# Optimization experiments

Hardware: AMD Instinct MI355X
Metric: run time of the kernel (lower is better)

Reference implementation:

```python
import jax, jax.numpy as jnp
import numpy as np

B, S, D, H, L, W, O = 4, 1024, 512, 8, 6, 64, 300
DH = D // H          # head dim = 64
R = 2 * W + 3        # rel_proj output dim = 131
EPS = 1e-6


def setup_inputs() -> dict:
    key = jax.random.key(0)
    ks = jax.random.split(key, 12)
    sc = 0.02
    x = jax.random.normal(ks[0], (B, S, D), jnp.float32)
    inp = {
        "x": x,
        "ln1_g": jnp.ones((L, D), jnp.float32),
        "ln1_b": jnp.zeros((L, D), jnp.float32),
        "qkv_w": jax.random.normal(ks[1], (L, D, 3 * D), jnp.float32) * sc,
        "qkv_b": jnp.zeros((L, 3 * D), jnp.float32),
        "rel_w": jax.random.normal(ks[2], (DH, R), jnp.float32) * sc,
        "rel_b": jnp.zeros((R,), jnp.float32),
        "ln2_g": jnp.ones((L, D), jnp.float32),
        "ln2_b": jnp.zeros((L, D), jnp.float32),
        "mlp_w1": jax.random.normal(ks[3], (L, D, 4 * D), jnp.float32) * sc,
        "mlp_b1": jnp.zeros((L, 4 * D), jnp.float32),
        "mlp_w2": jax.random.normal(ks[4], (L, 4 * D, D), jnp.float32) * sc,
        "mlp_b2": jnp.zeros((L, D), jnp.float32),
        "normf_g": jnp.ones((D,), jnp.float32),
        "normf_b": jnp.zeros((D,), jnp.float32),
        "head_w": jax.random.normal(ks[5], (D, O), jnp.float32) * sc,
        "head_b": jnp.zeros((O,), jnp.float32),
        "mask": jax.random.randint(ks[6], (B, O), 0, 2, jnp.int32),
    }
    return inp


def _layernorm(x, g, b):
    m = jnp.mean(x, axis=-1, keepdims=True)
    v = jnp.mean(jnp.square(x - m), axis=-1, keepdims=True)
    return (x - m) * jax.lax.rsqrt(v + EPS) * g + b


def _forward(x, ln1_g, ln1_b, qkv_w, qkv_b, rel_w, rel_b, ln2_g, ln2_b,
             mlp_w1, mlp_b1, mlp_w2, mlp_b2, normf_g, normf_b, head_w, head_b, mask):
    b, s, d = x.shape
    # clamped relative offsets, shifted to [0, 2W]; shape [s, s]
    ar = jnp.arange(s)
    offsets = jnp.clip(ar[None, :] - ar[:, None], -W, W) + W
    off_bh = jnp.broadcast_to(offsets[None, None], (b, H, s, s))
    scale = 1.0 / np.sqrt(D / H)  # = 1/sqrt(dh)

    def block(xc, lp):
        (l1g, l1b, qw, qb, l2g, l2b, w1, b1, w2, b2) = lp
        h = _layernorm(xc, l1g, l1b)
        qkv = (h @ qw + qb).reshape(b, s, H, 3 * DH)
        q, k, v = jnp.split(qkv, 3, axis=-1)            # [b,s,h,dh] each
        q = q.transpose(0, 2, 1, 3)                     # [b,h,s,dh]
        k = k.transpose(0, 2, 1, 3)
        v = v.transpose(0, 2, 1, 3)
        content = jnp.einsum('bhik,bhjk->bhij', q, k) * scale
        pos = q @ rel_w + rel_b                          # [b,h,s,R]
        pos_scores = jnp.take_along_axis(pos, off_bh, axis=-1)  # [b,h,s,s]
        attn = jax.nn.softmax(content + pos_scores, axis=-1)
        out = jnp.einsum('bhij,bhjk->bhik', attn, v)     # [b,h,s,dh]
        xc = xc + out.transpose(0, 2, 1, 3).reshape(b, s, d)
        h2 = _layernorm(xc, l2g, l2b)
        m = jax.nn.gelu(h2 @ w1 + b1, approximate=False) @ w2 + b2
        return xc + m, None

    layer_params = (ln1_g, ln1_b, qkv_w, qkv_b, ln2_g, ln2_b,
                    mlp_w1, mlp_b1, mlp_w2, mlp_b2)
    x, _ = jax.lax.scan(block, x, layer_params)
    x = _layernorm(x, normf_g, normf_b)[:, 0, :]         # CLS token
    logits = x @ head_w + head_b                          # [b, O]
    return jnp.where(mask == 0, -jnp.inf, logits)


def reference(x, ln1_g, ln1_b, qkv_w, qkv_b, rel_w, rel_b, ln2_g, ln2_b,
              mlp_w1, mlp_b1, mlp_w2, mlp_b2, normf_g, normf_b, head_w, head_b, mask):
    return _forward(x, ln1_g, ln1_b, qkv_w, qkv_b, rel_w, rel_b, ln2_g, ln2_b,
                    mlp_w1, mlp_b1, mlp_w2, mlp_b2, normf_g, normf_b, head_w, head_b, mask)
```

## Files before the change

### kernel.cpp

```cpp
#include <hip/hip_runtime.h>
#include <math.h>

#define B_  4
#define S_  1024
#define D_  512
#define H_  8
#define L_  6
#define W_  64
#define O_  300
#define DH_ 64
#define R_  131
#define R2_ 132

typedef __attribute__((ext_vector_type(8))) short bf16x8;
typedef __attribute__((ext_vector_type(4))) float f32x4;

#define SWZ(r) ((((r) ^ ((r) >> 3)) & 7) << 4)

__device__ __forceinline__ float gelu_f(float x) {
    return 0.5f * x * (1.0f + erff(x * 0.70710678118654752f));
}

__device__ __forceinline__ unsigned short f2bf(float f) {
    union { float f; unsigned u; } c; c.f = f;
    unsigned u = c.u;
    unsigned r = (u + 0x7fffu + ((u >> 16) & 1u)) >> 16;
    return (unsigned short)r;
}
__device__ __forceinline__ float bf2f(unsigned short u) {
    union { unsigned u; float f; } c; c.u = ((unsigned)u) << 16; return c.f;
}

__device__ __forceinline__ void gload_lds16(const void* g, void* l) {
    __builtin_amdgcn_global_load_lds(
        (const __attribute__((address_space(1))) unsigned int*)g,
        (__attribute__((address_space(3))) unsigned int*)l, 16, 0, 0);
}

__global__ __launch_bounds__(256) void ln_kernel(
    const float* __restrict__ x, const float* __restrict__ g,
    const float* __restrict__ b, unsigned short* __restrict__ y, int rows)
{
    int wave = threadIdx.x >> 6;
    int lane = threadIdx.x & 63;
    int row  = blockIdx.x * 4 + wave;
    if (row >= rows) return;
    const float* xr = x + (size_t)row * D_;
    float4 v0 = *(const float4*)(xr + lane * 4);
    float4 v1 = *(const float4*)(xr + 256 + lane * 4);

    float s = v0.x + v0.y + v0.z + v0.w + v1.x + v1.y + v1.z + v1.w;
    #pragma unroll
    for (int off = 32; off >= 1; off >>= 1) s += __shfl_xor(s, off);
    float mean = s * (1.0f / 512.0f);

    float a0 = v0.x - mean, a1 = v0.y - mean, a2 = v0.z - mean, a3 = v0.w - mean;
    float a4 = v1.x - mean, a5 = v1.y - mean, a6 = v1.z - mean, a7 = v1.w - mean;
    float vs = a0*a0 + a1*a1 + a2*a2 + a3*a3 + a4*a4 + a5*a5 + a6*a6 + a7*a7;
    #pragma unroll
    for (int off = 32; off >= 1; off >>= 1) vs += __shfl_xor(vs, off);
    float rstd = rsqrtf(vs * (1.0f / 512.0f) + 1e-6f);

    float4 g0 = *(const float4*)(g + lane * 4);
    float4 g1 = *(const float4*)(g + 256 + lane * 4);
    float4 b0 = *(const float4*)(b + lane * 4);
    float4 b1 = *(const float4*)(b + 256 + lane * 4);

    unsigned short* yr = y + (size_t)row * D_;
    ushort4 p0 = {f2bf(a0 * rstd * g0.x + b0.x), f2bf(a1 * rstd * g0.y + b0.y),
                  f2bf(a2 * rstd * g0.z + b0.z), f2bf(a3 * rstd * g0.w + b0.w)};
    ushort4 p1 = {f2bf(a4 * rstd * g1.x + b1.x), f2bf(a5 * rstd * g1.y + b1.y),
                  f2bf(a6 * rstd * g1.z + b1.z), f2bf(a7 * rstd * g1.w + b1.w)};
    *(ushort4*)(yr + lane * 4)       = p0;
    *(ushort4*)(yr + 256 + lane * 4) = p1;
}

__global__ __launch_bounds__(256) void tconv_kernel(
    const float* __restrict__ in, unsigned short* __restrict__ out, int K, int N)
{
    __shared__ float t[32][33];
    int tx = threadIdx.x & 31, ty = threadIdx.x >> 5;
    int n0 = blockIdx.x * 32, k0 = blockIdx.y * 32;
    #pragma unroll
    for (int j = 0; j < 4; ++j)
        t[ty + 8*j][tx] = in[(size_t)(k0 + ty + 8*j) * N + n0 + tx];
    __syncthreads();
    #pragma unroll
    for (int j = 0; j < 4; ++j)
        out[(size_t)(n0 + ty + 8*j) * K + k0 + tx] = f2bf(t[tx][ty + 8*j]);
}

__global__ __launch_bounds__(256) void relw_prep(
    const float* __restrict__ rel_w, unsigned short* __restrict__ relwT)
{
    for (int i = threadIdx.x; i < 144 * 64; i += 256) {
        int r = i >> 6, c = i & 63;
        relwT[i] = (r < R_) ? f2bf(rel_w[(size_t)c * R_ + r]) : (unsigned short)0;
    }
}

__global__ __launch_bounds__(256) void prep_all(
    const float* __restrict__ qkv_w, const float* __restrict__ mlp_w1,
    const float* __restrict__ mlp_w2, const float* __restrict__ rel_w,
    unsigned short* __restrict__ wTq_all, unsigned short* __restrict__ wT1_all,
    unsigned short* __restrict__ wT2_all, unsigned short* __restrict__ relwT)
{
    int bid = blockIdx.x;
    if (bid >= 16896) {
        for (int i = threadIdx.x; i < 144 * 64; i += 256) {
            int r = i >> 6, c = i & 63;
            relwT[i] = (r < R_) ? f2bf(rel_w[(size_t)c * R_ + r]) : (unsigned short)0;
        }
        return;
    }
    int l = bid / 2816, rr = bid - l * 2816;
    const float* in; unsigned short* out; int K, N, bx, by;
    if (rr < 768) {
        in = qkv_w + (size_t)l * 512 * 1536; out = wTq_all + (size_t)l * 1536 * 512;
        K = 512; N = 1536; bx = rr % 48; by = rr / 48;
    } else if (rr < 1792) {
        int r2 = rr - 768;
        in = mlp_w1 + (size_t)l * 512 * 2048; out = wT1_all + (size_t)l * 2048 * 512;
        K = 512; N = 2048; bx = r2 % 64; by = r2 / 64;
    } else {
        int r2 = rr - 1792;
        in = mlp_w2 + (size_t)l * 2048 * 512; out = wT2_all + (size_t)l * 512 * 2048;
        K = 2048; N = 512; bx = r2 % 16; by = r2 / 16;
    }
    __shared__ float t[32][33];
    int tx = threadIdx.x & 31, ty = threadIdx.x >> 5;
    int n0 = bx * 32, k0 = by * 32;
    #pragma unroll
    for (int j = 0; j < 4; ++j)
        t[ty + 8*j][tx] = in[(size_t)(k0 + ty + 8*j) * N + n0 + tx];
    __syncthreads();
    #pragma unroll
    for (int j = 0; j < 4; ++j)
        out[(size_t)(n0 + ty + 8*j) * K + k0 + tx] = f2bf(t[tx][ty + 8*j]);
}

template<int ACT, int OBF, int BM, int BN, int WM, int WN, int BK>
__global__ __launch_bounds__(256) void mfma_gemm(
    const unsigned short* __restrict__ A, const unsigned short* __restrict__ BT,
    const float* __restrict__ bias, const float* __restrict__ resid,
    void* __restrict__ Cout, int M, int N, int K)
{
    static_assert(WM * WN == 4, "4 waves");
    constexpr int MFR = BM / WM / 16;
    constexpr int NFR = BN / WN / 16;
    constexpr int TPR = BK / 8;
    constexpr int RPP = 256 / TPR;
    __shared__ __align__(16) unsigned short As[BM * BK];
    __shared__ __align__(16) unsigned short Bs[BN * BK];
    int tid  = threadIdx.x;
    int lane = tid & 63;
    int l15 = lane & 15, l4 = lane >> 4;
    int wid  = tid >> 6;
    int wave_m = (wid / WN) * (BM / WM);
    int wave_n = (wid % WN) * (BN / WN);

    int nwg = gridDim.x * gridDim.y;
    int bid0 = blockIdx.y * gridDim.x + blockIdx.x;
    int bid = (bid0 & 7) * (nwg >> 3) + (bid0 >> 3);
    int bm = (bid / gridDim.x) * BM, bn = (bid % gridDim.x) * BN;

    const f32x4 z4 = {0.f, 0.f, 0.f, 0.f};
    f32x4 acc[MFR][NFR];
    #pragma unroll
    for (int m = 0; m < MFR; ++m)
        #pragma unroll
        for (int n = 0; n < NFR; ++n) acc[m][n] = z4;

    int arow = tid / TPR;
    int acol8 = ((tid % TPR) ^ (arow & (TPR - 1))) * 8;
    const unsigned short* Ab = A  + (size_t)(bm + arow) * K + acol8;
    const unsigned short* Bb = BT + (size_t)(bn + arow) * K + acol8;
    unsigned short* Adst = As + tid * 8;
    unsigned short* Bdst = Bs + tid * 8;

    int swzA = l15 & (TPR - 1);
    const unsigned short* Afrag = As + (size_t)(wave_m + l15) * BK;
    const unsigned short* Bfrag = Bs + (size_t)(wave_n + l15) * BK;

    for (int k0 = 0; k0 < K; k0 += BK) {
        #pragma unroll
        for (int ch = 0; ch < BM / RPP; ++ch)
            gload_lds16(Ab + (size_t)ch * RPP * K + k0, Adst + ch * RPP * BK);
        #pragma unroll
        for (int ch = 0; ch < BN / RPP; ++ch)
            gload_lds16(Bb + (size_t)ch * RPP * K + k0, Bdst + ch * RPP * BK);
        __syncthreads();

        #pragma unroll
        for (int kk = 0; kk < BK / 32; ++kk) {
            int off8 = ((l4 + 4 * kk) ^ swzA) * 8;
            bf16x8 af[MFR], bfr[NFR];
            #pragma unroll
            for (int m = 0; m < MFR; ++m) af[m]  = *(const bf16x8*)(Afrag + m * 16 * BK + off8);
            #pragma unroll
            for (int n = 0; n < NFR; ++n) bfr[n] = *(const bf16x8*)(Bfrag + n * 16 * BK + off8);
            #pragma unroll
            for (int m = 0; m < MFR; ++m)
                #pragma unroll
                for (int n = 0; n < NFR; ++n)
                    acc[m][n] = __builtin_amdgcn_mfma_f32_16x16x32_bf16(af[m], bfr[n], acc[m][n], 0, 0, 0);
        }
        __syncthreads();
    }

    int r0 = bm + wave_m + (l4 * 4);
    int c0 = bn + wave_n + l15;
    #pragma unroll
    for (int m = 0; m < MFR; ++m) {
        #pragma unroll
        for (int n = 0; n < NFR; ++n) {
            int c = c0 + n * 16;
            float bv = bias[c];
            #pragma unroll
            for (int q = 0; q < 4; ++q) {
                int r = r0 + m * 16 + q;
                float v = acc[m][n][q] + bv;
                if (ACT == 1) v = gelu_f(v);
                if (resid) v += resid[(size_t)r * N + c];
                if (OBF) ((unsigned short*)Cout)[(size_t)r * N + c] = f2bf(v);
                else     ((float*)Cout)[(size_t)r * N + c] = v;
            }
        }
    }
}

__global__ __launch_bounds__(512, 2) void attn_mfma(
    const unsigned short* __restrict__ qkv,
    const unsigned short* __restrict__ relwT,
    const float* __restrict__ rel_b,
    float* __restrict__ xres)
{
    __shared__ __align__(16) unsigned char shm[49664];
    unsigned char* Klds  = shm;
    unsigned char* Vtlds = shm + 16384;
    unsigned short* pos16 = (unsigned short*)(shm + 32768);
    float* mergeO  = (float*)shm;
    float* mergeML = (float*)(shm + 17408);

    int tid = threadIdx.x, lane = tid & 63, w = tid >> 6;
    int l15 = lane & 15, l4 = lane >> 4;
    int wq = w & 3;
    int g  = w >> 2;
    int it0 = blockIdx.x * 64;
    int h = blockIdx.y, b = blockIdx.z;
    const float LOG2E = 1.4426950408889634f;
    const float SC = 0.125f * LOG2E;
    const float THR = 11.5441f;

    bf16x8 qa[2];
    {
        const unsigned short* qp = qkv + (size_t)(b * S_ + it0 + wq * 16 + l15) * 1536 + h * 192 + l4 * 8;
        qa[0] = *(const bf16x8*)(qp);
        qa[1] = *(const bf16x8*)(qp + 32);
    }

    if (g == 0) {
        #pragma unroll
        for (int n = 0; n < 9; ++n) {
            f32x4 pacc = {0.f, 0.f, 0.f, 0.f};
            #pragma unroll
            for (int ks = 0; ks < 2; ++ks) {
                bf16x8 bv = *(const bf16x8*)(relwT + (size_t)(16 * n + l15) * 64 + ks * 32 + l4 * 8);
                pacc = __builtin_amdgcn_mfma_f32_16x16x32_bf16(qa[ks], bv, pacc, 0, 0, 0);
            }
            int c = 16 * n + l15;
            if (c < R_) {
                float rb = rel_b[c];
                #pragma unroll
                for (int q = 0; q < 4; ++q)
                    pos16[(wq * 16 + l4 * 4 + q) * R2_ + c] = f2bf((pacc[q] + rb) * LOG2E);
            }
        }
    }
    __syncthreads();

    int rloc = wq * 16 + l15;
    int i_glob = it0 + rloc;
    float p_lo = bf2f(pos16[rloc * R2_ + 0]);
    float p_hi = bf2f(pos16[rloc * R2_ + 128]);

    int rf = tid >> 2, seg = tid & 3;
    int gk = rf >> 6, rr = rf & 63;
    const unsigned short* kbase = qkv + (size_t)(b * S_ + gk * 512 + rr) * 1536 + h * 192 + 64 + seg * 16;
    int kbyt = gk * 8192 + ((rr * 128 + seg * 32) ^ SWZ(rr));
    int pf = tid >> 3, seg8 = tid & 7;
    int gv = pf >> 5, pp = pf & 31;
    const unsigned short* vbase = qkv + (size_t)(b * S_ + gv * 512 + 2 * pp) * 1536 + h * 192 + 128 + seg8 * 8;
    bf16x8 kr0, kr1, vr0, vr1;
    kr0 = *(const bf16x8*)(kbase);
    kr1 = *(const bf16x8*)(kbase + 8);
    vr0 = *(const bf16x8*)(vbase);
    vr1 = *(const bf16x8*)(vbase + 1536);

    const f32x4 z4 = {0.f, 0.f, 0.f, 0.f};
    f32x4 oacc[4];
    #pragma unroll
    for (int n = 0; n < 4; ++n) oacc[n] = z4;
    float mrun_s = -INFINITY, lrun_s = 0.f;
    int wmin = it0 + wq * 16;
    unsigned char* Kw = Klds + g * 8192;
    unsigned char* Vw = Vtlds + g * 8192;

    int idx_lo = (l15 + 32 * (l4 & 1)) * 4;
    int idx_hi = idx_lo + 64;
    bool hi_n = (l4 >> 1) != 0;

    for (int t = 0; t < 8; ++t) {
        int jt0 = g * 512 + t * 64;
        __syncthreads();
        *(bf16x8*)(Klds + kbyt) = kr0;
        *(bf16x8*)(Klds + (kbyt ^ 16)) = kr1;
        #pragma unroll
        for (int i = 0; i < 8; ++i) {
            int dh = seg8 * 8 + i;
            unsigned v01 = (unsigned)(unsigned short)vr0[i] | ((unsigned)(unsigned short)vr1[i] << 16);
            *(unsigned*)(Vtlds + gv * 8192 + ((dh * 128 + pp * 4) ^ SWZ(dh))) = v01;
        }
        __syncthreads();
        if (t < 7) {
            const unsigned short* kp = kbase + (size_t)(t + 1) * 64 * 1536;
            kr0 = *(const bf16x8*)(kp);
            kr1 = *(const bf16x8*)(kp + 8);
            const unsigned short* vp = vbase + (size_t)(t + 1) * 64 * 1536;
            vr0 = *(const bf16x8*)(vp);
            vr1 = *(const bf16x8*)(vp + 1536);
        }

        f32x4 ssw[4];
        #pragma unroll
        for (int n = 0; n < 4; ++n) ssw[n] = z4;
        #pragma unroll
        for (int n = 0; n < 4; ++n) {
            int kvr = 16 * n + l15;
            #pragma unroll
            for (int ks = 0; ks < 2; ++ks) {
                bf16x8 ak = *(const bf16x8*)(Kw + ((kvr * 128 + ks * 64 + l4 * 16) ^ SWZ(kvr)));
                ssw[n] = __builtin_amdgcn_mfma_f32_16x16x32_bf16(ak, qa[ks], ssw[n], 0, 0, 0);
            }
        }

        float sv[4][4];
        bool left  = (jt0 + 63 < wmin - 64);
        bool right = (jt0 > wmin + 15 + 64);
        if (left || right) {
            float pc = left ? p_lo : p_hi;
            #pragma unroll
            for (int n = 0; n < 4; ++n)
                #pragma unroll
                for (int r = 0; r < 4; ++r) sv[n][r] = fmaf(ssw[n][r], SC, pc);
        } else {
            #pragma unroll
            for (int n = 0; n < 4; ++n)
                #pragma unroll
                for (int r = 0; r < 4; ++r) {
                    int j = jt0 + 16 * n + l4 * 4 + r;
                    int off = j - i_glob;
                    off = off < -64 ? -64 : (off > 64 ? 64 : off);
                    sv[n][r] = fmaf(ssw[n][r], SC, bf2f(pos16[rloc * R2_ + off + 64]));
                }
        }

        float a0 = fmaxf(fmaxf(sv[0][0], sv[0][1]), fmaxf(sv[0][2], sv[0][3]));
        float a1 = fmaxf(fmaxf(sv[1][0], sv[1][1]), fmaxf(sv[1][2], sv[1][3]));
        float a2 = fmaxf(fmaxf(sv[2][0], sv[2][1]), fmaxf(sv[2][2], sv[2][3]));
        float a3 = fmaxf(fmaxf(sv[3][0], sv[3][1]), fmaxf(sv[3][2], sv[3][3]));
        float mx = fmaxf(fmaxf(a0, a1), fmaxf(a2, a3));
        mx = fmaxf(mx, __shfl_xor(mx, 16));
        mx = fmaxf(mx, __shfl_xor(mx, 32));
        if (!__all(mx - mrun_s <= THR)) {
            float mnew = fmaxf(mrun_s, mx);
            float al = exp2f(mrun_s - mnew);
            mrun_s = mnew;
            lrun_s *= al;
            float alv0 = __shfl(al, l4 * 4 + 0);
            float alv1 = __shfl(al, l4 * 4 + 1);
            float alv2 = __shfl(al, l4 * 4 + 2);
            float alv3 = __shfl(al, l4 * 4 + 3);
            #pragma unroll
            for (int n = 0; n < 4; ++n) {
                oacc[n][0] *= alv0; oacc[n][1] *= alv1;
                oacc[n][2] *= alv2; oacc[n][3] *= alv3;
            }
        }
        float rs = 0.f;
        #pragma unroll
        for (int n = 0; n < 4; ++n)
            #pragma unroll
            for (int r = 0; r < 4; ++r) {
                float p = exp2f(sv[n][r] - mrun_s);
                sv[n][r] = p;
                rs += p;
            }
        rs += __shfl_xor(rs, 16);
        rs += __shfl_xor(rs, 32);
        lrun_s += rs;

        unsigned pkk[4][2];
        #pragma unroll
        for (int n = 0; n < 4; ++n) {
            asm("v_cvt_pk_bf16_f32 %0, %1, %2" : "=v"(pkk[n][0]) : "v"(sv[n][0]), "v"(sv[n][1]));
            asm("v_cvt_pk_bf16_f32 %0, %1, %2" : "=v"(pkk[n][1]) : "v"(sv[n][2]), "v"(sv[n][3]));
        }
        bf16x8 pa[2];
        #pragma unroll
        for (int ks = 0; ks < 2; ++ks) {
            unsigned wrd[4];
            #pragma unroll
            for (int ww = 0; ww < 4; ++ww) {
                int srcidx = (ww >> 1) ? idx_hi : idx_lo;
                unsigned vlo = (unsigned)__builtin_amdgcn_ds_bpermute(srcidx, (int)pkk[2 * ks + 0][ww & 1]);
                unsigned vhi = (unsigned)__builtin_amdgcn_ds_bpermute(srcidx, (int)pkk[2 * ks + 1][ww & 1]);
                wrd[ww] = hi_n ? vhi : vlo;
            }
            union { unsigned u[4]; bf16x8 v; } cvt;
            cvt.u[0] = wrd[0]; cvt.u[1] = wrd[1]; cvt.u[2] = wrd[2]; cvt.u[3] = wrd[3];
            pa[ks] = cvt.v;
        }

        #pragma unroll
        for (int n = 0; n < 4; ++n) {
            int dh = 16 * n + l15;
            #pragma unroll
            for (int ks = 0; ks < 2; ++ks) {
                bf16x8 bv = *(const bf16x8*)(Vw + ((dh * 128 + ks * 64 + l4 * 16) ^ SWZ(dh)));
                oacc[n] = __builtin_amdgcn_mfma_f32_16x16x32_bf16(pa[ks], bv, oacc[n], 0, 0, 0);
            }
        }
    }

    __syncthreads();
    if (g == 1) {
        #pragma unroll
        for (int n = 0; n < 4; ++n)
            #pragma unroll
            for (int r = 0; r < 4; ++r)
                mergeO[(wq * 16 + l4 * 4 + r) * 68 + 16 * n + l15] = oacc[n][r];
        if (lane < 16) {
            mergeML[rloc * 2 + 0] = mrun_s;
            mergeML[rloc * 2 + 1] = lrun_s;
        }
    }
    __syncthreads();
    if (g == 0) {
        float mb = mergeML[rloc * 2 + 0];
        float lb = mergeML[rloc * 2 + 1];
        float M  = fmaxf(mrun_s, mb);
        float fa = exp2f(mrun_s - M);
        float fb = exp2f(mb - M);
        float inv = 1.0f / (lrun_s * fa + lb * fb);
        float A_s = fa * inv, B_s = fb * inv;
        float Av[4], Bv[4];
        #pragma unroll
        for (int r = 0; r < 4; ++r) {
            Av[r] = __shfl(A_s, l4 * 4 + r);
            Bv[r] = __shfl(B_s, l4 * 4 + r);
        }
        #pragma unroll
        for (int r = 0; r < 4; ++r) {
            int row = wq * 16 + l4 * 4 + r;
            float* xp = xres + (size_t)(b * S_ + it0 + row) * D_ + h * DH_;
            #pragma unroll
            for (int n = 0; n < 4; ++n)
                xp[16 * n + l15] += oacc[n][r] * Av[r] + mergeO[row * 68 + 16 * n + l15] * Bv[r];
        }
    }
}

__global__ __launch_bounds__(256) void head_kernel(
    const float* __restrict__ xc, const float* __restrict__ gf,
    const float* __restrict__ bfp, const float* __restrict__ hw,
    const float* __restrict__ hbias, const int* __restrict__ mask,
    float* __restrict__ out)
{
    __shared__ float a[4][512];
    __shared__ float part[4][64][4];
    int tid = threadIdx.x;
    int wv = tid >> 6, lane = tid & 63;
    {
        const float* xr = xc + (size_t)wv * S_ * D_;
        float4 v0 = *(const float4*)(xr + lane * 4);
        float4 v1 = *(const float4*)(xr + 256 + lane * 4);
        float s = v0.x + v0.y + v0.z + v0.w + v1.x + v1.y + v1.z + v1.w;
        #pragma unroll
        for (int off = 32; off >= 1; off >>= 1) s += __shfl_xor(s, off);
        float mean = s * (1.0f / 512.0f);
        float c0 = v0.x - mean, c1 = v0.y - mean, c2 = v0.z - mean, c3 = v0.w - mean;
        float c4 = v1.x - mean, c5 = v1.y - mean, c6 = v1.z - mean, c7 = v1.w - mean;
        float vs = c0*c0 + c1*c1 + c2*c2 + c3*c3 + c4*c4 + c5*c5 + c6*c6 + c7*c7;
        #pragma unroll
        for (int off = 32; off >= 1; off >>= 1) vs += __shfl_xor(vs, off);
        float rstd = rsqrtf(vs * (1.0f / 512.0f) + 1e-6f);
        float4 g0 = *(const float4*)(gf + lane * 4);
        float4 g1 = *(const float4*)(gf + 256 + lane * 4);
        float4 b0 = *(const float4*)(bfp + lane * 4);
        float4 b1 = *(const float4*)(bfp + 256 + lane * 4);
        a[wv][lane * 4 + 0] = c0 * rstd * g0.x + b0.x;
        a[wv][lane * 4 + 1] = c1 * rstd * g0.y + b0.y;
        a[wv][lane * 4 + 2] = c2 * rstd * g0.z + b0.z;
        a[wv][lane * 4 + 3] = c3 * rstd * g0.w + b0.w;
        a[wv][256 + lane * 4 + 0] = c4 * rstd * g1.x + b1.x;
        a[wv][256 + lane * 4 + 1] = c5 * rstd * g1.y + b1.y;
        a[wv][256 + lane * 4 + 2] = c6 * rstd * g1.z + b1.z;
        a[wv][256 + lane * 4 + 3] = c7 * rstd * g1.w + b1.w;
    }
    __syncthreads();

    int cl = tid & 63;
    int c  = blockIdx.x * 64 + cl;
    int ks = tid >> 6;
    float ac[4] = {0.f, 0.f, 0.f, 0.f};
    if (c < O_) {
        const float* wp = hw + (size_t)(ks * 128) * O_ + c;
        #pragma unroll 8
        for (int k = 0; k < 128; ++k) {
            float wvv = wp[(size_t)k * O_];
            int kk = ks * 128 + k;
            ac[0] = fmaf(a[0][kk], wvv, ac[0]);
            ac[1] = fmaf(a[1][kk], wvv, ac[1]);
            ac[2] = fmaf(a[2][kk], wvv, ac[2]);
            ac[3] = fmaf(a[3][kk], wvv, ac[3]);
        }
    }
    #pragma unroll
    for (int bb = 0; bb < 4; ++bb) part[ks][cl][bb] = ac[bb];
    __syncthreads();
    if (ks == 0 && c < O_) {
        float hbv = hbias[c];
        #pragma unroll
        for (int bb = 0; bb < 4; ++bb) {
            float v = part[0][cl][bb] + part[1][cl][bb] + part[2][cl][bb] + part[3][cl][bb] + hbv;
            out[bb * O_ + c] = (mask[bb * O_ + c] == 0) ? -1e30f : v;
        }
    }
}

extern "C" void kernel_launch(void* const* d_in, const int* in_sizes, int n_in,
                              void* d_out, int out_size, void* d_ws, size_t ws_size,
                              hipStream_t stream) {
    const float* x      = (const float*)d_in[0];
    const float* ln1_g  = (const float*)d_in[1];
    const float* ln1_b  = (const float*)d_in[2];
    const float* qkv_w  = (const float*)d_in[3];
    const float* qkv_b  = (const float*)d_in[4];
    const float* rel_w  = (const float*)d_in[5];
    const float* rel_b  = (const float*)d_in[6];
    const float* ln2_g  = (const float*)d_in[7];
    const float* ln2_b  = (const float*)d_in[8];
    const float* mlp_w1 = (const float*)d_in[9];
    const float* mlp_b1 = (const float*)d_in[10];
    const float* mlp_w2 = (const float*)d_in[11];
    const float* mlp_b2 = (const float*)d_in[12];
    const float* normf_g = (const float*)d_in[13];
    const float* normf_b = (const float*)d_in[14];
    const float* head_w  = (const float*)d_in[15];
    const float* head_b  = (const float*)d_in[16];
    const int*   mask    = (const int*)d_in[17];
    float* out = (float*)d_out;
    float* ws  = (float*)d_ws;

    const int NR = B_ * S_;
    dim3 blk(256);

    float* x_cur = ws;
    float* reg2  = ws + 2097152;
    unsigned short* qkv16 = (unsigned short*)reg2;
    unsigned short* midb  = (unsigned short*)reg2;

    hipMemcpyAsync(x_cur, x, (size_t)NR * D_ * sizeof(float),
                   hipMemcpyDeviceToDevice, stream);

    bool hoist = ws_size >= (size_t)15995392 * 4;

    if (hoist) {
        unsigned short* hb      = (unsigned short*)(ws + 6291456);
        unsigned short* wTq_all = (unsigned short*)(ws + 7340032);
        unsigned short* wT1_all = (unsigned short*)(ws + 9699328);
        unsigned short* wT2_all = (unsigned short*)(ws + 12845056);
        unsigned short* relwT   = (unsigned short*)(ws + 15990784);

        prep_all<<<16897, blk, 0, stream>>>(qkv_w, mlp_w1, mlp_w2, rel_w,
                                            wTq_all, wT1_all, wT2_all, relwT);

        for (int l = 0; l < L_; ++l) {
            ln_kernel<<<NR / 4, blk, 0, stream>>>(x_cur, ln1_g + l * D_, ln1_b + l * D_, hb, NR);
            mfma_gemm<0, 1, 128, 64, 4, 1, 64><<<dim3(24, 32), blk, 0, stream>>>(
                hb, wTq_all + (size_t)l * 1536 * 512, qkv_b + (size_t)l * 3 * D_,
                nullptr, qkv16, NR, 3 * D_, D_);
            attn_mfma<<<dim3(S_ / 64, H_, B_), dim3(512), 0, stream>>>(qkv16, relwT, rel_b, x_cur);
            ln_kernel<<<NR / 4, blk, 0, stream>>>(x_cur, ln2_g + l * D_, ln2_b + l * D_, hb, NR);
            mfma_gemm<1, 1, 128, 64, 4, 1, 64><<<dim3(32, 32), blk, 0, stream>>>(
                hb, wT1_all + (size_t)l * 2048 * 512, mlp_b1 + (size_t)l * 4 * D_,
                nullptr, midb, NR, 4 * D_, D_);
            mfma_gemm<0, 0, 64, 64, 2, 2, 64><<<dim3(8, 64), blk, 0, stream>>>(
                midb, wT2_all + (size_t)l * 512 * 2048, mlp_b2 + (size_t)l * D_,
                x_cur, x_cur, NR, D_, 4 * D_);
        }
        head_kernel<<<dim3(5), blk, 0, stream>>>(x_cur, normf_g, normf_b,
                                                 head_w, head_b, mask, out);
    } else {
        float* wregs = ws + 6291456;
        unsigned short* hb    = (unsigned short*)wregs;
        unsigned short* wTq   = (unsigned short*)(wregs + 1048576);
        unsigned short* wT1   = (unsigned short*)(wregs + 1441792);
        unsigned short* wT2   = (unsigned short*)(wregs + 1966080);
        unsigned short* relwT = (unsigned short*)(ws + 10616832);

        relw_prep<<<1, blk, 0, stream>>>(rel_w, relwT);
        for (int l = 0; l < L_; ++l) {
            ln_kernel<<<NR / 4, blk, 0, stream>>>(x_cur, ln1_g + l * D_, ln1_b + l * D_, hb, NR);
            tconv_kernel<<<dim3(48, 16), blk, 0, stream>>>(
                qkv_w + (size_t)l * D_ * 3 * D_, wTq, D_, 3 * D_);
            mfma_gemm<0, 1, 128, 64, 4, 1, 64><<<dim3(24, 32), blk, 0, stream>>>(
                hb, wTq, qkv_b + (size_t)l * 3 * D_, nullptr, qkv16, NR, 3 * D_, D_);
            attn_mfma<<<dim3(S_ / 64, H_, B_), dim3(512), 0, stream>>>(qkv16, relwT, rel_b, x_cur);
            ln_kernel<<<NR / 4, blk, 0, stream>>>(x_cur, ln2_g + l * D_, ln2_b + l * D_, hb, NR);
            tconv_kernel<<<dim3(64, 16), blk, 0, stream>>>(
                mlp_w1 + (size_t)l * D_ * 4 * D_, wT1, D_, 4 * D_);
            mfma_gemm<1, 1, 128, 64, 4, 1, 64><<<dim3(32, 32), blk, 0, stream>>>(
                hb, wT1, mlp_b1 + (size_t)l * 4 * D_, nullptr, midb, NR, 4 * D_, D_);
            tconv_kernel<<<dim3(16, 64), blk, 0, stream>>>(
                mlp_w2 + (size_t)l * 4 * D_ * D_, wT2, 4 * D_, D_);
            mfma_gemm<0, 0, 64, 64, 2, 2, 64><<<dim3(8, 64), blk, 0, stream>>>(
                midb, wT2, mlp_b2 + (size_t)l * D_, x_cur, x_cur, NR, D_, 4 * D_);
        }
        head_kernel<<<dim3(5), blk, 0, stream>>>(x_cur, normf_g, normf_b,
                                                 head_w, head_b, mask, out);
    }
}
```

Before: 631.6 us.

## Double-buffer LDS in MFMA GEMM to overlap global loads with compute

Doubles the shared-memory tiles in the bf16 MFMA GEMM and prefetches the next two K-tiles with direct global-to-LDS loads. Each iteration waits on a partial vmcnt, loads all fragments into registers, then issues the next stage's loads before running the MFMAs. The goal is to hide global memory latency behind matrix math instead of stalling on a full barrier every K step. In exchange it uses twice the LDS and more fragment registers, which may lower occupancy, and the hand-coded vmcnt values only cover certain load counts.

```diff
diff --git a/kernel.cpp b/kernel.cpp
--- a/kernel.cpp
+++ b/kernel.cpp
@@ -150,8 +150,11 @@
     constexpr int NFR = BN / WN / 16;
     constexpr int TPR = BK / 8;
     constexpr int RPP = 256 / TPR;
-    __shared__ __align__(16) unsigned short As[BM * BK];
-    __shared__ __align__(16) unsigned short Bs[BN * BK];
+    constexpr int ACH = BM / RPP, BCH = BN / RPP;
+    constexpr int LOADS = ACH + BCH;
+    constexpr int KK = BK / 32;
+    __shared__ __align__(16) unsigned short As[2 * BM * BK];
+    __shared__ __align__(16) unsigned short Bs[2 * BN * BK];
     int tid  = threadIdx.x;
     int lane = tid & 63;
     int l15 = lane & 15, l4 = lane >> 4;
@@ -182,30 +185,60 @@
     const unsigned short* Afrag = As + (size_t)(wave_m + l15) * BK;
     const unsigned short* Bfrag = Bs + (size_t)(wave_n + l15) * BK;
 
-    for (int k0 = 0; k0 < K; k0 += BK) {
-        #pragma unroll
-        for (int ch = 0; ch < BM / RPP; ++ch)
-            gload_lds16(Ab + (size_t)ch * RPP * K + k0, Adst + ch * RPP * BK);
-        #pragma unroll
-        for (int ch = 0; ch < BN / RPP; ++ch)
-            gload_lds16(Bb + (size_t)ch * RPP * K + k0, Bdst + ch * RPP * BK);
-        __syncthreads();
-
-        #pragma unroll
-        for (int kk = 0; kk < BK / 32; ++kk) {
-            int off8 = ((l4 + 4 * kk) ^ swzA) * 8;
-            bf16x8 af[MFR], bfr[NFR];
-            #pragma unroll
-            for (int m = 0; m < MFR; ++m) af[m]  = *(const bf16x8*)(Afrag + m * 16 * BK + off8);
-            #pragma unroll
-            for (int n = 0; n < NFR; ++n) bfr[n] = *(const bf16x8*)(Bfrag + n * 16 * BK + off8);
+    const int NT = K / BK;
+
+    auto STAGE = [&](int buf, int k0) {
+        #pragma unroll
+        for (int ch = 0; ch < ACH; ++ch)
+            gload_lds16(Ab + (size_t)ch * RPP * K + k0, Adst + buf * BM * BK + ch * RPP * BK);
+        #pragma unroll
+        for (int ch = 0; ch < BCH; ++ch)
+            gload_lds16(Bb + (size_t)ch * RPP * K + k0, Bdst + buf * BN * BK + ch * RPP * BK);
+    };
+
+    STAGE(0, 0);
+    STAGE(1, BK);
+
+    int off8[KK];
+    #pragma unroll
+    for (int kk = 0; kk < KK; ++kk) off8[kk] = ((l4 + 4 * kk) ^ swzA) * 8;
+
+    for (int t = 0; t < NT; ++t) {
+        int cur = t & 1;
+        if (t + 1 < NT) {
+            if constexpr (LOADS == 6) asm volatile("s_waitcnt vmcnt(6)" ::: "memory");
+            else if constexpr (LOADS == 4) asm volatile("s_waitcnt vmcnt(4)" ::: "memory");
+            else asm volatile("s_waitcnt vmcnt(0)" ::: "memory");
+        } else {
+            asm volatile("s_waitcnt vmcnt(0)" ::: "memory");
+        }
+        __builtin_amdgcn_s_barrier();
+        asm volatile("" ::: "memory");
+
+        const unsigned short* Af = Afrag + cur * BM * BK;
+        const unsigned short* Bf = Bfrag + cur * BN * BK;
+        bf16x8 af[KK][MFR], bfr[KK][NFR];
+        #pragma unroll
+        for (int kk = 0; kk < KK; ++kk) {
+            #pragma unroll
+            for (int m = 0; m < MFR; ++m) af[kk][m]  = *(const bf16x8*)(Af + m * 16 * BK + off8[kk]);
+            #pragma unroll
+            for (int n = 0; n < NFR; ++n) bfr[kk][n] = *(const bf16x8*)(Bf + n * 16 * BK + off8[kk]);
+        }
+        asm volatile("s_waitcnt lgkmcnt(0)" ::: "memory");
+        __builtin_amdgcn_sched_barrier(0);
+        __builtin_amdgcn_s_barrier();
+        asm volatile("" ::: "memory");
+
+        if (t + 2 < NT) STAGE(cur, (t + 2) * BK);
+
+        #pragma unroll
+        for (int kk = 0; kk < KK; ++kk)
             #pragma unroll
             for (int m = 0; m < MFR; ++m)
                 #pragma unroll
                 for (int n = 0; n < NFR; ++n)
-                    acc[m][n] = __builtin_amdgcn_mfma_f32_16x16x32_bf16(af[m], bfr[n], acc[m][n], 0, 0, 0);
-        }
-        __syncthreads();
+                    acc[m][n] = __builtin_amdgcn_mfma_f32_16x16x32_bf16(af[kk][m], bfr[kk][n], acc[m][n], 0, 0, 0);
     }
 
     int r0 = bm + wave_m + (l4 * 4);
```

New measurement: 624.5 us. About the same (-1.1%).
